# Optimization experiments

Measured on AMD Instinct MI355X. Metric: run time of the kernel, lower is better.

## Reference

```python
import jax, jax.numpy as jnp
import numpy as np

V, D, T_BLK, H, HS = 50257, 512, 2048, 8, 64
B, T = 2, 2048


def setup_inputs() -> dict:
    key = jax.random.key(0)
    ks = jax.random.split(key, 12)
    s = 0.02
    return {
        "idx": jax.random.randint(ks[0], (B, T), 0, V),
        "targets": jax.random.randint(ks[1], (B, T), 0, V),
        "tok_emb": jax.random.normal(ks[2], (V, D), jnp.float32) * s,
        "pos_emb": jax.random.normal(ks[3], (T_BLK, D), jnp.float32) * s,
        "wq": jax.random.normal(ks[4], (H, D, HS), jnp.float32) * s,
        "wk": jax.random.normal(ks[5], (H, D, HS), jnp.float32) * s,
        "wv": jax.random.normal(ks[6], (H, D, HS), jnp.float32) * s,
        "w1": jax.random.normal(ks[7], (D, D), jnp.float32) * s,
        "b1": jnp.zeros((D,), jnp.float32),
        "w_head": jax.random.normal(ks[8], (D, V), jnp.float32) * s,
        "b_head": jnp.zeros((V,), jnp.float32),
    }


def _forward(idx, targets, tok_emb, pos_emb, wq, wk, wv, w1, b1, w_head, b_head):
    b, t = idx.shape
    x = tok_emb[idx] + pos_emb[:t]                        # [B,T,D]
    # batched per-head QKV (equivalent to the per-head Linear loop)
    q = jnp.einsum("btd,hde->bhte", x, wq)                # [B,H,T,hs]
    k = jnp.einsum("btd,hde->bhte", x, wk)
    v = jnp.einsum("btd,hde->bhte", x, wv)
    scores = jnp.einsum("bhte,bhse->bhts", q, k) / jnp.sqrt(jnp.float32(HS))
    causal = jnp.tril(jnp.ones((t, t), bool))
    scores = jnp.where(causal, scores, -jnp.inf)
    weights = jax.nn.softmax(scores, axis=-1)
    att = jnp.einsum("bhts,bhse->bhte", weights, v)       # [B,H,T,hs]
    att = att.transpose(0, 2, 1, 3).reshape(b, t, H * HS)  # head-concat order
    x_ff = jax.nn.relu(att @ w1 + b1)                      # [B,T,D]
    logits = x_ff @ w_head + b_head                        # [B,T,V]
    logp = jax.nn.log_softmax(logits, axis=-1)
    loss = -jnp.mean(jnp.take_along_axis(logp, targets[..., None], axis=-1))
    return logits, loss


def reference(idx, targets, tok_emb, pos_emb, wq, wk, wv, w1, b1, w_head, b_head):
    return _forward(idx, targets, tok_emb, pos_emb, wq, wk, wv, w1, b1, w_head, b_head)
```

## Files before the change

### kernel.cpp

```cpp
#include <hip/hip_runtime.h>
#include <hip/hip_bf16.h>
#include <stdint.h>

#define V_SZ   50257
#define NPAD   50432
#define NT_HEAD 197
#define D_SZ   512
#define HS_SZ  64
#define H_N    8
#define T_SZ   2048
#define ROWS   4096

typedef __bf16 bf16x8 __attribute__((ext_vector_type(8)));
typedef __bf16 bf16x4 __attribute__((ext_vector_type(4)));
typedef float  f32x4  __attribute__((ext_vector_type(4)));

__device__ __forceinline__ void gload_lds16(const void* g, void* l) {
  auto gp = (const __attribute__((address_space(1))) uint32_t*)(uintptr_t)g;
  auto lp = (__attribute__((address_space(3))) uint32_t*)(uintptr_t)l;
  __builtin_amdgcn_global_load_lds(gp, lp, 16, 0, 0);
}

__global__ __launch_bounds__(256) void k_embed(const int* __restrict__ idx,
    const float* __restrict__ tok, const float* __restrict__ pos,
    __bf16* __restrict__ xb) {
  const int row = blockIdx.x;
  const int tpos = row & (T_SZ - 1);
  const int tokid = idx[row];
  const int d = threadIdx.x * 2;
  float2 tv = *(const float2*)(tok + (size_t)tokid * D_SZ + d);
  float2 pv = *(const float2*)(pos + (size_t)tpos * D_SZ + d);
  __bf16* o = xb + (size_t)row * D_SZ + d;
  o[0] = (__bf16)(tv.x + pv.x);
  o[1] = (__bf16)(tv.y + pv.y);
}

__global__ __launch_bounds__(256) void k_prep_wqkv(const float* __restrict__ wq,
    const float* __restrict__ wk, const float* __restrict__ wv, __bf16* __restrict__ dst) {
  const int id = blockIdx.x * 256 + threadIdx.x;
  const int n = id >> 9, dd = id & 511;
  const int mi = n >> 9, rem = n & 511, h = rem >> 6, e = rem & 63;
  const float* src = (mi == 0) ? wq : ((mi == 1) ? wk : wv);
  dst[id] = (__bf16)src[((size_t)h * D_SZ + dd) * HS_SZ + e];
}

__global__ __launch_bounds__(256) void k_prep_w1(const float* __restrict__ w1,
                                                 __bf16* __restrict__ dst) {
  const int id = blockIdx.x * 256 + threadIdx.x;
  const int n = id >> 9, kk = id & 511;
  dst[id] = (__bf16)w1[(size_t)kk * D_SZ + n];
}

__global__ void k_prep_wh(const float* __restrict__ wh, __bf16* __restrict__ dst) {
  __shared__ float tile[32][33];
  const int n0 = blockIdx.x * 32, d0 = blockIdx.y * 32;
  const int tx = threadIdx.x, ty = threadIdx.y;
  #pragma unroll
  for (int i = 0; i < 4; ++i) {
    int dd = d0 + ty + i * 8, n = n0 + tx;
    tile[ty + i * 8][tx] = (n < V_SZ) ? wh[(size_t)dd * V_SZ + n] : 0.f;
  }
  __syncthreads();
  #pragma unroll
  for (int i = 0; i < 4; ++i) {
    int n = n0 + ty + i * 8, dd = d0 + tx;
    dst[(size_t)n * D_SZ + dd] = (__bf16)tile[tx][ty + i * 8];
  }
}

template <int EPI>
__global__ __launch_bounds__(256) void k_gemm(const __bf16* __restrict__ A,
    const __bf16* __restrict__ Bt, const float* __restrict__ bias,
    __bf16* __restrict__ outH, __bf16* __restrict__ outK, __bf16* __restrict__ outV) {
  __shared__ __bf16 As[128 * 32];
  __shared__ __bf16 Bs[128 * 32];
  const int t = threadIdx.x, lane = t & 63, w = t >> 6;
  const int wr = w >> 1, wc = w & 1;
  const int m0 = blockIdx.x * 128, n0 = blockIdx.y * 128;
  const int srow = lane >> 2, k8 = (lane & 3) * 8;

  f32x4 zero = {0.f, 0.f, 0.f, 0.f};
  f32x4 acc[4][4];
  #pragma unroll
  for (int mm = 0; mm < 4; ++mm)
    #pragma unroll
    for (int nn = 0; nn < 4; ++nn) acc[mm][nn] = zero;

  const __bf16* Ag = A  + (size_t)(m0 + w * 16 + srow) * D_SZ + k8;
  const __bf16* Bg = Bt + (size_t)(n0 + w * 16 + srow) * D_SZ + k8;
  char* AsB = (char*)As + w * 1024;
  char* BsB = (char*)Bs + w * 1024;
  const int kslot = (lane >> 4) * 8;
  const int arow = wr * 64 + (lane & 15);
  const int brow = wc * 64 + (lane & 15);

  for (int kt = 0; kt < 16; ++kt) {
    const int k0 = kt * 32;
    gload_lds16(Ag + k0,             AsB);
    gload_lds16(Ag + 64 * D_SZ + k0, AsB + 4096);
    gload_lds16(Bg + k0,             BsB);
    gload_lds16(Bg + 64 * D_SZ + k0, BsB + 4096);
    __syncthreads();

    bf16x8 af[4], bfr[4];
    #pragma unroll
    for (int mm = 0; mm < 4; ++mm)
      af[mm] = *(const bf16x8*)(As + (arow + mm * 16) * 32 + kslot);
    #pragma unroll
    for (int nn = 0; nn < 4; ++nn)
      bfr[nn] = *(const bf16x8*)(Bs + (brow + nn * 16) * 32 + kslot);
    #pragma unroll
    for (int mm = 0; mm < 4; ++mm)
      #pragma unroll
      for (int nn = 0; nn < 4; ++nn)
        acc[mm][nn] = __builtin_amdgcn_mfma_f32_16x16x32_bf16(af[mm], bfr[nn], acc[mm][nn], 0, 0, 0);
    __syncthreads();
  }

  const int lrow = (lane >> 4) * 4, lcol = lane & 15;
  #pragma unroll
  for (int mm = 0; mm < 4; ++mm) {
    #pragma unroll
    for (int nn = 0; nn < 4; ++nn) {
      const int grow0 = m0 + wr * 64 + mm * 16 + lrow;
      const int gcol  = n0 + wc * 64 + nn * 16 + lcol;
      if (EPI == 0) {
        const int mi = gcol >> 9, rem = gcol & 511, hh = rem >> 6, e = rem & 63;
        const int bb = grow0 >> 11, tt0 = grow0 & 2047;
        const int bhh = bb * H_N + hh;
        if (mi == 2) {
          bf16x4 pk = { (__bf16)acc[mm][nn][0], (__bf16)acc[mm][nn][1],
                        (__bf16)acc[mm][nn][2], (__bf16)acc[mm][nn][3] };
          *(bf16x4*)(outV + ((size_t)bhh * HS_SZ + e) * T_SZ + tt0) = pk;
        } else {
          __bf16* dq = (mi == 0 ? outH : outK) + ((size_t)bhh * T_SZ + tt0) * HS_SZ + e;
          const float sc = (mi == 0) ? 0.125f : 1.f;
          #pragma unroll
          for (int j = 0; j < 4; ++j) dq[(size_t)j * HS_SZ] = (__bf16)(acc[mm][nn][j] * sc);
        }
      } else {
        #pragma unroll
        for (int j = 0; j < 4; ++j) {
          float xv = acc[mm][nn][j] + bias[gcol];
          outH[(size_t)(grow0 + j) * D_SZ + gcol] = (__bf16)(xv > 0.f ? xv : 0.f);
        }
      }
    }
  }
}

__global__ __launch_bounds__(512, 2) void k_ghead(const __bf16* __restrict__ A,
    const __bf16* __restrict__ Bt, const float* __restrict__ bias,
    float* __restrict__ logits, float2* __restrict__ part) {
  __shared__ char lds[131072];
  const int t = threadIdx.x, lane = t & 63, w = t >> 6;
  const int wr = w >> 2, wc = w & 3;
  const int m0 = blockIdx.x * 256, n0 = blockIdx.y * 256;
  const int r8 = lane >> 3, cc = lane & 7;
  const int lm = lane & 15, g = lane >> 4, l7 = lane & 7;
  const int csw = (cc ^ r8) << 4;
  const int srow8 = w * 8 + r8;

  f32x4 acc[8][4];
  #pragma unroll
  for (int mm = 0; mm < 8; ++mm)
    #pragma unroll
    for (int nn = 0; nn < 4; ++nn) acc[mm][nn] = f32x4{0.f, 0.f, 0.f, 0.f};

  const char* Ab = (const char*)A  + (size_t)m0 * (D_SZ * 2);
  const char* Bb = (const char*)Bt + (size_t)n0 * (D_SZ * 2);

  auto STAGE = [&](int buf, int kt) {
    char* Al = lds + buf * 65536;
    char* Bl = Al + 32768;
    const char* Asrc = Ab + kt * 128;
    const char* Bsrc = Bb + kt * 128;
    #pragma unroll
    for (int i = 0; i < 4; ++i) {
      gload_lds16(Asrc + (size_t)(i * 64 + srow8) * 1024 + csw, Al + (i * 64 + w * 8) * 128);
      gload_lds16(Bsrc + (size_t)(i * 64 + srow8) * 1024 + csw, Bl + (i * 64 + w * 8) * 128);
    }
  };

  STAGE(0, 0);
  STAGE(1, 1);
  asm volatile("s_waitcnt vmcnt(8)" ::: "memory");
  __builtin_amdgcn_s_barrier();
  asm volatile("" ::: "memory");

  for (int kt = 0; kt < 8; ++kt) {
    const char* Al = lds + (kt & 1) * 65536;
    const char* Bl = Al + 32768;
    #pragma unroll
    for (int kh = 0; kh < 2; ++kh) {
      const int ch = ((g + kh * 4) ^ l7) << 4;
      bf16x8 a[8], b[4];
      #pragma unroll
      for (int mm = 0; mm < 8; ++mm)
        a[mm] = *(const bf16x8*)(Al + (wr * 128 + mm * 16 + lm) * 128 + ch);
      #pragma unroll
      for (int nn = 0; nn < 4; ++nn)
        b[nn] = *(const bf16x8*)(Bl + (wc * 64 + nn * 16 + lm) * 128 + ch);
      #pragma unroll
      for (int mm = 0; mm < 8; ++mm)
        #pragma unroll
        for (int nn = 0; nn < 4; ++nn)
          acc[mm][nn] = __builtin_amdgcn_mfma_f32_16x16x32_bf16(a[mm], b[nn], acc[mm][nn], 0, 0, 0);
    }
    if (kt == 7) break;
    __builtin_amdgcn_s_barrier();
    asm volatile("" ::: "memory");
    if (kt < 6) {
      STAGE(kt & 1, kt + 2);
      asm volatile("s_waitcnt vmcnt(8)" ::: "memory");
    } else {
      asm volatile("s_waitcnt vmcnt(0)" ::: "memory");
    }
    __builtin_amdgcn_s_barrier();
    asm volatile("" ::: "memory");
  }
  __syncthreads();

  float* tr   = (float*)lds;
  float* redS = tr + 32 * 260;
  const int colL = wc * 64 + lm;
  float bj[4]; int vok[4];
  #pragma unroll
  for (int nn = 0; nn < 4; ++nn) {
    const int gc = n0 + colL + nn * 16;
    vok[nn] = (gc < V_SZ);
    bj[nn] = vok[nn] ? bias[gc] : 0.f;
  }
  const int r32s = t >> 4, c16 = t & 15;
  #pragma unroll
  for (int mm = 0; mm < 8; ++mm) {
    if (mm) __syncthreads();
    float sj[4];
    #pragma unroll
    for (int j = 0; j < 4; ++j) {
      const int r32 = wr * 16 + g * 4 + j;
      float s = 0.f;
      #pragma unroll
      for (int nn = 0; nn < 4; ++nn) {
        const float v = acc[mm][nn][j] + bj[nn];
        tr[r32 * 260 + colL + nn * 16] = v;
        if (vok[nn]) s += __expf(v);
      }
      sj[j] = s;
    }
    #pragma unroll
    for (int j = 0; j < 4; ++j) {
      float s = sj[j];
      s += __shfl_xor(s, 1); s += __shfl_xor(s, 2);
      s += __shfl_xor(s, 4); s += __shfl_xor(s, 8);
      if (lm == 0) redS[(wr * 128 + mm * 16 + g * 4 + j) * 4 + wc] = s;
    }
    __syncthreads();
    const int grow = m0 + (r32s >> 4) * 128 + mm * 16 + (r32s & 15);
    float* gp = logits + (size_t)grow * V_SZ;
    #pragma unroll
    for (int i = 0; i < 4; ++i) {
      const int c4 = c16 + 16 * i;
      const int gc0 = n0 + c4 * 4;
      f32x4 vv = *(const f32x4*)(tr + r32s * 260 + c4 * 4);
      if (gc0 + 3 < V_SZ) {
        *(f32x4*)(gp + gc0) = vv;
      } else {
        if (gc0     < V_SZ) gp[gc0]     = vv.x;
        if (gc0 + 1 < V_SZ) gp[gc0 + 1] = vv.y;
        if (gc0 + 2 < V_SZ) gp[gc0 + 2] = vv.z;
        if (gc0 + 3 < V_SZ) gp[gc0 + 3] = vv.w;
      }
    }
  }
  __syncthreads();
  if (t < 256) {
    const float S = redS[t * 4] + redS[t * 4 + 1] + redS[t * 4 + 2] + redS[t * 4 + 3];
    part[(size_t)(m0 + t) * NT_HEAD + blockIdx.y] = float2{0.f, S};
  }
}

__global__ __launch_bounds__(256) void k_attn(const __bf16* __restrict__ qbf,
    const __bf16* __restrict__ kbf, const __bf16* __restrict__ vbf,
    __bf16* __restrict__ xatt) {
  const int qt = 31 - blockIdx.x;
  const int bh = blockIdx.y;
  const int b = bh >> 3, h = bh & 7;
  const int t = threadIdx.x, lane = t & 63, w = t >> 6;
  const int qr = lane & 15, g = lane >> 4, r7 = qr & 7;
  __shared__ __bf16 Klds[64 * 64];
  __shared__ __bf16 Vt[64 * 64];
  __shared__ __bf16 Plds[4][16 * 72];

  const int qglob = qt * 64 + w * 16 + qr;
  const __bf16* qrow_g = qbf + ((size_t)bh * T_SZ + qglob) * HS_SZ + g * 8;
  const bf16x8 qf0 = *(const bf16x8*)(qrow_g);
  const bf16x8 qf1 = *(const bf16x8*)(qrow_g + 32);

  f32x4 att[4];
  #pragma unroll
  for (int n = 0; n < 4; ++n) att[n] = f32x4{0.f, 0.f, 0.f, 0.f};
  float m = -3.0e38f, l = 0.f;

  const char* Kg = (const char*)(kbf + (size_t)bh * T_SZ * HS_SZ);
  const char* Vg = (const char*)(vbf + (size_t)bh * HS_SZ * T_SZ);
  const int r8 = lane >> 3, cc = lane & 7;
  const int csw = ((cc ^ r8) << 4);

  for (int kt = 0; kt <= qt; ++kt) {
    if (kt) __syncthreads();
    {
      const char* ks = Kg + (size_t)(kt * 64 + w * 16) * 128;
      gload_lds16(ks + r8 * 128 + csw,        (char*)Klds + w * 2048);
      gload_lds16(ks + 1024 + r8 * 128 + csw, (char*)Klds + w * 2048 + 1024);
      const char* vs = Vg + (size_t)(w * 16) * (T_SZ * 2) + kt * 128;
      gload_lds16(vs + r8 * (T_SZ * 2) + csw,                   (char*)Vt + w * 2048);
      gload_lds16(vs + (8 + r8) * (T_SZ * 2) + csw,             (char*)Vt + w * 2048 + 1024);
    }
    __syncthreads();

    const bool diag = (kt == qt);
    f32x4 acc[4];
    #pragma unroll
    for (int a = 0; a < 4; ++a) {
      if (diag && a > w) {
        acc[a] = f32x4{-3.0e38f, -3.0e38f, -3.0e38f, -3.0e38f};
      } else {
        const char* kb = (const char*)Klds + (a * 16 + qr) * 128;
        bf16x8 ka0 = *(const bf16x8*)(kb + ((g ^ r7) << 4));
        bf16x8 ka1 = *(const bf16x8*)(kb + (((g + 4) ^ r7) << 4));
        f32x4 z = {0.f, 0.f, 0.f, 0.f};
        z = __builtin_amdgcn_mfma_f32_16x16x32_bf16(ka0, qf0, z, 0, 0, 0);
        z = __builtin_amdgcn_mfma_f32_16x16x32_bf16(ka1, qf1, z, 0, 0, 0);
        acc[a] = z;
      }
    }
    if (diag) {
      #pragma unroll
      for (int a = 0; a < 4; ++a)
        #pragma unroll
        for (int j = 0; j < 4; ++j)
          if (a * 16 + g * 4 + j > w * 16 + qr) acc[a][j] = -3.0e38f;
    }

    float mloc = -3.0e38f;
    #pragma unroll
    for (int a = 0; a < 4; ++a)
      #pragma unroll
      for (int j = 0; j < 4; ++j) mloc = fmaxf(mloc, acc[a][j]);
    mloc = fmaxf(mloc, __shfl_xor(mloc, 16));
    mloc = fmaxf(mloc, __shfl_xor(mloc, 32));
    const float newm = fmaxf(m, mloc);
    const float alpha = __expf(m - newm);
    float lloc = 0.f;
    #pragma unroll
    for (int a = 0; a < 4; ++a) {
      float p0 = __expf(acc[a][0] - newm);
      float p1 = __expf(acc[a][1] - newm);
      float p2 = __expf(acc[a][2] - newm);
      float p3 = __expf(acc[a][3] - newm);
      lloc += (p0 + p1) + (p2 + p3);
      bf16x4 pw = { (__bf16)p0, (__bf16)p1, (__bf16)p2, (__bf16)p3 };
      *(bf16x4*)((char*)&Plds[w][0] + qr * 144 + (a * 16 + g * 4) * 2) = pw;
    }
    lloc += __shfl_xor(lloc, 16);
    lloc += __shfl_xor(lloc, 32);
    l = l * alpha + lloc;
    m = newm;

    #pragma unroll
    for (int j = 0; j < 4; ++j) {
      const float aj = __shfl(alpha, g * 4 + j);
      #pragma unroll
      for (int n = 0; n < 4; ++n) att[n][j] *= aj;
    }

    #pragma unroll
    for (int c = 0; c < 2; ++c) {
      bf16x8 pa = *(const bf16x8*)((const char*)&Plds[w][0] + qr * 144 + c * 64 + g * 16);
      #pragma unroll
      for (int n = 0; n < 4; ++n) {
        const int vrow = n * 16 + qr;
        bf16x8 vb = *(const bf16x8*)((const char*)Vt + vrow * 128 + (((c * 4 + g) ^ r7) << 4));
        att[n] = __builtin_amdgcn_mfma_f32_16x16x32_bf16(pa, vb, att[n], 0, 0, 0);
      }
    }
  }

  #pragma unroll
  for (int j = 0; j < 4; ++j) {
    const float lj = __shfl(l, g * 4 + j);
    const float inv = 1.f / lj;
    const int row = qt * 64 + w * 16 + g * 4 + j;
    __bf16* orow = xatt + ((size_t)(b * T_SZ + row)) * D_SZ + h * HS_SZ + qr;
    #pragma unroll
    for (int n = 0; n < 4; ++n) orow[n * 16] = (__bf16)(att[n][j] * inv);
  }
}

__global__ __launch_bounds__(256) void k_lsemerge(const float2* __restrict__ part,
                                                  float* __restrict__ lse) {
  const int row = blockIdx.x * 4 + (threadIdx.x >> 6);
  const int lane = threadIdx.x & 63;
  const float2* pr = part + (size_t)row * NT_HEAD;
  float M = -3.0e38f, S = 0.f;
  for (int i = lane; i < NT_HEAD; i += 64) {
    float2 p = pr[i];
    float nm = fmaxf(M, p.x);
    S = S * __expf(M - nm) + p.y * __expf(p.x - nm);
    M = nm;
  }
  #pragma unroll
  for (int off = 1; off < 64; off <<= 1) {
    float Mo = __shfl_xor(M, off), So = __shfl_xor(S, off);
    float nm = fmaxf(M, Mo);
    S = S * __expf(M - nm) + So * __expf(Mo - nm);
    M = nm;
  }
  if (lane == 0) lse[row] = M + __logf(S);
}

__global__ __launch_bounds__(256) void k_loss(const float* __restrict__ logits,
    const float* __restrict__ lse, const int* __restrict__ tgt,
    float* __restrict__ outloss) {
  float acc = 0.f;
  for (int r = threadIdx.x; r < ROWS; r += 256)
    acc += lse[r] - logits[(size_t)r * V_SZ + tgt[r]];
  #pragma unroll
  for (int off = 32; off > 0; off >>= 1) acc += __shfl_down(acc, off);
  __shared__ float pw[4];
  if ((threadIdx.x & 63) == 0) pw[threadIdx.x >> 6] = acc;
  __syncthreads();
  if (threadIdx.x == 0) outloss[0] = (pw[0] + pw[1] + pw[2] + pw[3]) * (1.f / ROWS);
}

extern "C" void kernel_launch(void* const* d_in, const int* in_sizes, int n_in,
                              void* d_out, int out_size, void* d_ws, size_t ws_size,
                              hipStream_t stream) {
  const int*   idx = (const int*)d_in[0];
  const int*   tgt = (const int*)d_in[1];
  const float* tok = (const float*)d_in[2];
  const float* pos = (const float*)d_in[3];
  const float* wq  = (const float*)d_in[4];
  const float* wk  = (const float*)d_in[5];
  const float* wv  = (const float*)d_in[6];
  const float* w1  = (const float*)d_in[7];
  const float* b1  = (const float*)d_in[8];
  const float* wh  = (const float*)d_in[9];
  const float* bh  = (const float*)d_in[10];

  float* logits = (float*)d_out;
  float* lossp  = logits + (size_t)ROWS * V_SZ;

  char* ws = (char*)d_ws;
  __bf16* xb   = (__bf16*)(ws + 0);
  __bf16* Bqkv = (__bf16*)(ws + (4u  << 20));
  __bf16* B1t  = (__bf16*)(ws + (11u << 19));
  __bf16* qbf  = (__bf16*)(ws + (6u  << 20));
  __bf16* kbf  = (__bf16*)(ws + (10u << 20));
  __bf16* vbf  = (__bf16*)(ws + (14u << 20));
  float2* part = (float2*)(ws + 0);
  float*  lse  = (float*) (ws + (20u << 20));
  __bf16* xatt = (__bf16*)(ws + (30u << 20));
  __bf16* Aff  = (__bf16*)(ws + (34u << 20));
  __bf16* Wht  = (__bf16*)(ws + (38u << 20));

  k_embed    <<<ROWS, 256, 0, stream>>>(idx, tok, pos, xb);
  k_prep_wqkv<<<3072, 256, 0, stream>>>(wq, wk, wv, Bqkv);
  k_prep_w1  <<<1024, 256, 0, stream>>>(w1, B1t);
  k_prep_wh  <<<dim3(NPAD / 32, 16), dim3(32, 8), 0, stream>>>(wh, Wht);

  k_gemm<0><<<dim3(32, 12),  256, 0, stream>>>(xb,   Bqkv, nullptr, qbf, kbf, vbf);
  k_attn   <<<dim3(32, 16),  256, 0, stream>>>(qbf, kbf, vbf, xatt);
  k_gemm<1><<<dim3(32, 4),   256, 0, stream>>>(xatt, B1t,  b1,  Aff, nullptr, nullptr);
  k_ghead  <<<dim3(16, NT_HEAD), 512, 0, stream>>>(Aff, Wht, bh, logits, part);

  k_lsemerge<<<ROWS / 4, 256, 0, stream>>>(part, lse);
  k_loss    <<<1,        256, 0, stream>>>(logits, lse, tgt, lossp);
}
```

Baseline: 565.0 us.

## Permute head weight columns so logits store directly from MFMA registers

The prep kernel now reorders the transposed head weight rows within each 64-column group. As a result, each lane's four MFMA accumulator columns map to four consecutive global vocabulary columns. The GEMM epilogue can then write logits as f32x4 straight from registers, dropping the per-tile LDS transpose and the barriers around it. The cost is less regular row-to-row write grouping, and possibly misaligned 16-byte stores because the V-sized row stride is odd.

```diff
diff --git a/kernel.cpp b/kernel.cpp
--- a/kernel.cpp
+++ b/kernel.cpp
@@ -64,7 +64,8 @@
   #pragma unroll
   for (int i = 0; i < 4; ++i) {
     int n = n0 + ty + i * 8, dd = d0 + tx;
-    dst[(size_t)n * D_SZ + dd] = (__bf16)tile[tx][ty + i * 8];
+    int np = (n & ~63) | ((n & 3) * 16 + ((n & 63) >> 2));
+    dst[(size_t)np * D_SZ + dd] = (__bf16)tile[tx][ty + i * 8];
   }
 }
 
@@ -221,62 +222,50 @@
   }
   __syncthreads();
 
-  float* tr   = (float*)lds;
-  float* redS = tr + 32 * 260;
-  const int colL = wc * 64 + lm;
-  float bj[4]; int vok[4];
+  float* redS = (float*)lds;
+  const int cbase = n0 + wc * 64 + lm * 4;
+  float bj[4];
   #pragma unroll
   for (int nn = 0; nn < 4; ++nn) {
-    const int gc = n0 + colL + nn * 16;
-    vok[nn] = (gc < V_SZ);
-    bj[nn] = vok[nn] ? bias[gc] : 0.f;
-  }
-  const int r32s = t >> 4, c16 = t & 15;
+    const int c = cbase + nn;
+    bj[nn] = (c < V_SZ) ? bias[c] : 0.f;
+  }
+  const bool full4 = (cbase + 3 < V_SZ);
   #pragma unroll
   for (int mm = 0; mm < 8; ++mm) {
-    if (mm) __syncthreads();
-    float sj[4];
     #pragma unroll
     for (int j = 0; j < 4; ++j) {
-      const int r32 = wr * 16 + g * 4 + j;
       float s = 0.f;
       #pragma unroll
-      for (int nn = 0; nn < 4; ++nn) {
-        const float v = acc[mm][nn][j] + bj[nn];
-        tr[r32 * 260 + colL + nn * 16] = v;
-        if (vok[nn]) s += __expf(v);
-      }
-      sj[j] = s;
-    }
-    #pragma unroll
-    for (int j = 0; j < 4; ++j) {
-      float s = sj[j];
+      for (int nn = 0; nn < 4; ++nn)
+        if (cbase + nn < V_SZ) s += __expf(acc[mm][nn][j] + bj[nn]);
       s += __shfl_xor(s, 1); s += __shfl_xor(s, 2);
       s += __shfl_xor(s, 4); s += __shfl_xor(s, 8);
       if (lm == 0) redS[(wr * 128 + mm * 16 + g * 4 + j) * 4 + wc] = s;
-    }
-    __syncthreads();
-    const int grow = m0 + (r32s >> 4) * 128 + mm * 16 + (r32s & 15);
-    float* gp = logits + (size_t)grow * V_SZ;
-    #pragma unroll
-    for (int i = 0; i < 4; ++i) {
-      const int c4 = c16 + 16 * i;
-      const int gc0 = n0 + c4 * 4;
-      f32x4 vv = *(const f32x4*)(tr + r32s * 260 + c4 * 4);
-      if (gc0 + 3 < V_SZ) {
-        *(f32x4*)(gp + gc0) = vv;
-      } else {
-        if (gc0     < V_SZ) gp[gc0]     = vv.x;
-        if (gc0 + 1 < V_SZ) gp[gc0 + 1] = vv.y;
-        if (gc0 + 2 < V_SZ) gp[gc0 + 2] = vv.z;
-        if (gc0 + 3 < V_SZ) gp[gc0 + 3] = vv.w;
-      }
     }
   }
   __syncthreads();
   if (t < 256) {
     const float S = redS[t * 4] + redS[t * 4 + 1] + redS[t * 4 + 2] + redS[t * 4 + 3];
     part[(size_t)(m0 + t) * NT_HEAD + blockIdx.y] = float2{0.f, S};
+  }
+  #pragma unroll
+  for (int mm = 0; mm < 8; ++mm) {
+    const int row0 = m0 + wr * 128 + mm * 16 + g * 4;
+    #pragma unroll
+    for (int j = 0; j < 4; ++j) {
+      float* gp = logits + (size_t)(row0 + j) * V_SZ + cbase;
+      f32x4 v4 = { acc[mm][0][j] + bj[0], acc[mm][1][j] + bj[1],
+                   acc[mm][2][j] + bj[2], acc[mm][3][j] + bj[3] };
+      if (full4) {
+        *(f32x4*)gp = v4;
+      } else {
+        if (cbase     < V_SZ) gp[0] = v4.x;
+        if (cbase + 1 < V_SZ) gp[1] = v4.y;
+        if (cbase + 2 < V_SZ) gp[2] = v4.z;
+        if (cbase + 3 < V_SZ) gp[3] = v4.w;
+      }
+    }
   }
 }
 
```

Measured after the change: 623.0 us. 10.3% more time.

## Run LM-head GEMM in FP8 e4m3 with scaled activations and weights

Applied to the files above, without the earlier changes.

Quantizes the FFN output activations and the transposed head weights to FP8 e4m3, each scaled by 256, and switches the head GEMM to fp8 MFMA. The result is rescaled by 1/65536 before the bias is added. This halves operand bytes and LDS use, which allows a smaller LDS footprint and higher occupancy (launch bounds 512,4) and is meant to cut the MFMA and memory cost of the dominant head GEMM. The cost is accuracy: FP8 quantization error in the logits may exceed the tolerance, and the log-sum-exp epilogue and logits write are unchanged.

```diff
diff --git a/kernel.cpp b/kernel.cpp
--- a/kernel.cpp
+++ b/kernel.cpp
@@ -1,5 +1,6 @@
 #include <hip/hip_runtime.h>
 #include <hip/hip_bf16.h>
+#include <hip/hip_fp8.h>
 #include <stdint.h>
 
 #define V_SZ   50257
@@ -14,6 +15,11 @@
 typedef __bf16 bf16x8 __attribute__((ext_vector_type(8)));
 typedef __bf16 bf16x4 __attribute__((ext_vector_type(4)));
 typedef float  f32x4  __attribute__((ext_vector_type(4)));
+
+__device__ __forceinline__ unsigned char to_fp8(float x) {
+  __hip_fp8_e4m3 t(x);
+  return t.__x;
+}
 
 __device__ __forceinline__ void gload_lds16(const void* g, void* l) {
   auto gp = (const __attribute__((address_space(1))) uint32_t*)(uintptr_t)g;
@@ -51,7 +57,7 @@
   dst[id] = (__bf16)w1[(size_t)kk * D_SZ + n];
 }
 
-__global__ void k_prep_wh(const float* __restrict__ wh, __bf16* __restrict__ dst) {
+__global__ void k_prep_wh(const float* __restrict__ wh, unsigned char* __restrict__ dst) {
   __shared__ float tile[32][33];
   const int n0 = blockIdx.x * 32, d0 = blockIdx.y * 32;
   const int tx = threadIdx.x, ty = threadIdx.y;
@@ -64,14 +70,14 @@
   #pragma unroll
   for (int i = 0; i < 4; ++i) {
     int n = n0 + ty + i * 8, dd = d0 + tx;
-    dst[(size_t)n * D_SZ + dd] = (__bf16)tile[tx][ty + i * 8];
+    dst[(size_t)n * D_SZ + dd] = to_fp8(tile[tx][ty + i * 8] * 256.f);
   }
 }
 
 template <int EPI>
 __global__ __launch_bounds__(256) void k_gemm(const __bf16* __restrict__ A,
     const __bf16* __restrict__ Bt, const float* __restrict__ bias,
-    __bf16* __restrict__ outH, __bf16* __restrict__ outK, __bf16* __restrict__ outV) {
+    unsigned char* __restrict__ outA8, __bf16* __restrict__ outK, __bf16* __restrict__ outV) {
   __shared__ __bf16 As[128 * 32];
   __shared__ __bf16 Bs[128 * 32];
   const int t = threadIdx.x, lane = t & 63, w = t >> 6;
@@ -133,7 +139,7 @@
                         (__bf16)acc[mm][nn][2], (__bf16)acc[mm][nn][3] };
           *(bf16x4*)(outV + ((size_t)bhh * HS_SZ + e) * T_SZ + tt0) = pk;
         } else {
-          __bf16* dq = (mi == 0 ? outH : outK) + ((size_t)bhh * T_SZ + tt0) * HS_SZ + e;
+          __bf16* dq = (mi == 0 ? (__bf16*)outA8 : outK) + ((size_t)bhh * T_SZ + tt0) * HS_SZ + e;
           const float sc = (mi == 0) ? 0.125f : 1.f;
           #pragma unroll
           for (int j = 0; j < 4; ++j) dq[(size_t)j * HS_SZ] = (__bf16)(acc[mm][nn][j] * sc);
@@ -142,24 +148,25 @@
         #pragma unroll
         for (int j = 0; j < 4; ++j) {
           float xv = acc[mm][nn][j] + bias[gcol];
-          outH[(size_t)(grow0 + j) * D_SZ + gcol] = (__bf16)(xv > 0.f ? xv : 0.f);
+          xv = (xv > 0.f ? xv : 0.f) * 256.f;
+          outA8[(size_t)(grow0 + j) * D_SZ + gcol] = to_fp8(xv);
         }
       }
     }
   }
 }
 
-__global__ __launch_bounds__(512, 2) void k_ghead(const __bf16* __restrict__ A,
-    const __bf16* __restrict__ Bt, const float* __restrict__ bias,
+__global__ __launch_bounds__(512, 4) void k_ghead(const unsigned char* __restrict__ A,
+    const unsigned char* __restrict__ Bt, const float* __restrict__ bias,
     float* __restrict__ logits, float2* __restrict__ part) {
-  __shared__ char lds[131072];
+  __shared__ char lds[65536];
   const int t = threadIdx.x, lane = t & 63, w = t >> 6;
   const int wr = w >> 2, wc = w & 3;
   const int m0 = blockIdx.x * 256, n0 = blockIdx.y * 256;
-  const int r8 = lane >> 3, cc = lane & 7;
-  const int lm = lane & 15, g = lane >> 4, l7 = lane & 7;
-  const int csw = (cc ^ r8) << 4;
-  const int srow8 = w * 8 + r8;
+  const int lm = lane & 15, g = lane >> 4;
+  const int l3 = lm & 3;
+  const int r2 = lane >> 2, c2 = lane & 3;
+  const int csw2 = (c2 ^ (r2 & 3)) << 4;
 
   f32x4 acc[8][4];
   #pragma unroll
@@ -167,52 +174,51 @@
     #pragma unroll
     for (int nn = 0; nn < 4; ++nn) acc[mm][nn] = f32x4{0.f, 0.f, 0.f, 0.f};
 
-  const char* Ab = (const char*)A  + (size_t)m0 * (D_SZ * 2);
-  const char* Bb = (const char*)Bt + (size_t)n0 * (D_SZ * 2);
+  const unsigned char* Ab = A  + (size_t)m0 * D_SZ;
+  const unsigned char* Bb = Bt + (size_t)n0 * D_SZ;
 
   auto STAGE = [&](int buf, int kt) {
-    char* Al = lds + buf * 65536;
-    char* Bl = Al + 32768;
-    const char* Asrc = Ab + kt * 128;
-    const char* Bsrc = Bb + kt * 128;
-    #pragma unroll
-    for (int i = 0; i < 4; ++i) {
-      gload_lds16(Asrc + (size_t)(i * 64 + srow8) * 1024 + csw, Al + (i * 64 + w * 8) * 128);
-      gload_lds16(Bsrc + (size_t)(i * 64 + srow8) * 1024 + csw, Bl + (i * 64 + w * 8) * 128);
+    char* Al = lds + buf * 32768;
+    #pragma unroll
+    for (int i = 0; i < 2; ++i) {
+      const int rbase = i * 128 + w * 16;
+      gload_lds16(Ab + (size_t)(rbase + r2) * D_SZ + kt * 64 + csw2, Al + rbase * 64);
+      gload_lds16(Bb + (size_t)(rbase + r2) * D_SZ + kt * 64 + csw2, Al + 16384 + rbase * 64);
     }
   };
 
   STAGE(0, 0);
   STAGE(1, 1);
-  asm volatile("s_waitcnt vmcnt(8)" ::: "memory");
+  asm volatile("s_waitcnt vmcnt(4)" ::: "memory");
   __builtin_amdgcn_s_barrier();
   asm volatile("" ::: "memory");
 
   for (int kt = 0; kt < 8; ++kt) {
-    const char* Al = lds + (kt & 1) * 65536;
-    const char* Bl = Al + 32768;
+    const char* Al = lds + (kt & 1) * 32768;
+    const char* Bl = Al + 16384;
     #pragma unroll
     for (int kh = 0; kh < 2; ++kh) {
-      const int ch = ((g + kh * 4) ^ l7) << 4;
-      bf16x8 a[8], b[4];
+      const int s = kh * 4 + g;
+      const int off = (((s >> 1) ^ l3) << 4) + ((s & 1) << 3);
+      long a[8], b[4];
       #pragma unroll
       for (int mm = 0; mm < 8; ++mm)
-        a[mm] = *(const bf16x8*)(Al + (wr * 128 + mm * 16 + lm) * 128 + ch);
+        a[mm] = *(const long*)(Al + (wr * 128 + mm * 16 + lm) * 64 + off);
       #pragma unroll
       for (int nn = 0; nn < 4; ++nn)
-        b[nn] = *(const bf16x8*)(Bl + (wc * 64 + nn * 16 + lm) * 128 + ch);
+        b[nn] = *(const long*)(Bl + (wc * 64 + nn * 16 + lm) * 64 + off);
       #pragma unroll
       for (int mm = 0; mm < 8; ++mm)
         #pragma unroll
         for (int nn = 0; nn < 4; ++nn)
-          acc[mm][nn] = __builtin_amdgcn_mfma_f32_16x16x32_bf16(a[mm], b[nn], acc[mm][nn], 0, 0, 0);
+          acc[mm][nn] = __builtin_amdgcn_mfma_f32_16x16x32_fp8_fp8(a[mm], b[nn], acc[mm][nn], 0, 0, 0);
     }
     if (kt == 7) break;
     __builtin_amdgcn_s_barrier();
     asm volatile("" ::: "memory");
     if (kt < 6) {
       STAGE(kt & 1, kt + 2);
-      asm volatile("s_waitcnt vmcnt(8)" ::: "memory");
+      asm volatile("s_waitcnt vmcnt(4)" ::: "memory");
     } else {
       asm volatile("s_waitcnt vmcnt(0)" ::: "memory");
     }
@@ -221,6 +227,7 @@
   }
   __syncthreads();
 
+  const float SC = 1.f / 65536.f;
   float* tr   = (float*)lds;
   float* redS = tr + 32 * 260;
   const int colL = wc * 64 + lm;
@@ -242,7 +249,7 @@
       float s = 0.f;
       #pragma unroll
       for (int nn = 0; nn < 4; ++nn) {
-        const float v = acc[mm][nn][j] + bj[nn];
+        const float v = acc[mm][nn][j] * SC + bj[nn];
         tr[r32 * 260 + colL + nn * 16] = v;
         if (vok[nn]) s += __expf(v);
       }
@@ -462,18 +469,18 @@
   float2* part = (float2*)(ws + 0);
   float*  lse  = (float*) (ws + (20u << 20));
   __bf16* xatt = (__bf16*)(ws + (30u << 20));
-  __bf16* Aff  = (__bf16*)(ws + (34u << 20));
-  __bf16* Wht  = (__bf16*)(ws + (38u << 20));
+  unsigned char* Aff8 = (unsigned char*)(ws + (34u << 20));
+  unsigned char* Wht8 = (unsigned char*)(ws + (38u << 20));
 
   k_embed    <<<ROWS, 256, 0, stream>>>(idx, tok, pos, xb);
   k_prep_wqkv<<<3072, 256, 0, stream>>>(wq, wk, wv, Bqkv);
   k_prep_w1  <<<1024, 256, 0, stream>>>(w1, B1t);
-  k_prep_wh  <<<dim3(NPAD / 32, 16), dim3(32, 8), 0, stream>>>(wh, Wht);
-
-  k_gemm<0><<<dim3(32, 12),  256, 0, stream>>>(xb,   Bqkv, nullptr, qbf, kbf, vbf);
+  k_prep_wh  <<<dim3(NPAD / 32, 16), dim3(32, 8), 0, stream>>>(wh, Wht8);
+
+  k_gemm<0><<<dim3(32, 12),  256, 0, stream>>>(xb,   Bqkv, nullptr, (unsigned char*)qbf, kbf, vbf);
   k_attn   <<<dim3(32, 16),  256, 0, stream>>>(qbf, kbf, vbf, xatt);
-  k_gemm<1><<<dim3(32, 4),   256, 0, stream>>>(xatt, B1t,  b1,  Aff, nullptr, nullptr);
-  k_ghead  <<<dim3(16, NT_HEAD), 512, 0, stream>>>(Aff, Wht, bh, logits, part);
+  k_gemm<1><<<dim3(32, 4),   256, 0, stream>>>(xatt, B1t,  b1,  Aff8, nullptr, nullptr);
+  k_ghead  <<<dim3(16, NT_HEAD), 512, 0, stream>>>(Aff8, Wht8, bh, logits, part);
 
   k_lsemerge<<<ROWS / 4, 256, 0, stream>>>(part, lse);
   k_loss    <<<1,        256, 0, stream>>>(logits, lse, tgt, lossp);
```

Result: slower. 1.282 ms (+127.0%).
